# Performance work log

Measured on AMD Instinct MI355X. Metric: run time of the kernel, lower is better.

## Reference

```python
import jax, jax.numpy as jnp
import numpy as np

WD = 8        # window_dim
E = 32        # embedding_dim
D = E * WD * WD   # attention_dim = 2048
NH = 8        # num_heads (SwinTransformer default)
B, H, W = 16, 64, 64
NW = (H // WD) * (W // WD)  # 64 windows
FF = 4 * D


def _partition(x):
    # 'b (vp vw) (hp hw) e -> b (vw hw) (vp hp e)', vp=hp=WD (patches are the OUTER factor)
    b, h, w, e = x.shape
    vw, hw = h // WD, w // WD
    x = x.reshape(b, WD, vw, WD, hw, e)
    x = x.transpose(0, 2, 4, 1, 3, 5)           # b vw hw vp hp e
    return x.reshape(b, vw * hw, WD * WD * e)   # [B, NW, D]


def _layer_norm(x, g, b, eps=1e-5):
    m = jnp.mean(x, axis=-1, keepdims=True)
    v = jnp.mean(jnp.square(x - m), axis=-1, keepdims=True)
    return (x - m) * jax.lax.rsqrt(v + eps) * g + b


def setup_inputs() -> dict:
    key = jax.random.key(0)
    ks = jax.random.split(key, 8)
    s = 0.02  # weight scale to keep activations sane at D=2048
    return {
        'embeddings': jax.random.normal(ks[0], (B, H, W, E), jnp.float32),
        'ln1_g': jnp.ones((D,), jnp.float32),
        'ln1_b': jnp.zeros((D,), jnp.float32),
        'wq': jax.random.normal(ks[1], (D, D), jnp.float32) * s,
        'bq': jnp.zeros((D,), jnp.float32),
        'wk': jax.random.normal(ks[2], (D, D), jnp.float32) * s,
        'bk': jnp.zeros((D,), jnp.float32),
        'wv': jax.random.normal(ks[3], (D, D), jnp.float32) * s,
        'bv': jnp.zeros((D,), jnp.float32),
        'pos_bias': jnp.zeros((NW, NW), jnp.float32),  # source discards the randn Parameter; bias is zeros
        'ln2_g': jnp.ones((D,), jnp.float32),
        'ln2_b': jnp.zeros((D,), jnp.float32),
        'w1': jax.random.normal(ks[4], (D, FF), jnp.float32) * s,
        'b1': jnp.zeros((FF,), jnp.float32),
        'w2': jax.random.normal(ks[5], (FF, D), jnp.float32) * s,
        'b2': jnp.zeros((D,), jnp.float32),
    }


def reference(embeddings, ln1_g, ln1_b, wq, bq, wk, bk, wv, bv, pos_bias,
              ln2_g, ln2_b, w1, b1, w2, b2):
    windows = _partition(embeddings)                       # [B, NW, D]
    x = _layer_norm(windows, ln1_g, ln1_b)
    hd = D // NH

    def heads(y):  # [B, NW, D] -> [B, NH, NW, hd]  (heads are outer factor)
        return y.reshape(B, NW, NH, hd).transpose(0, 2, 1, 3)

    q = heads(x @ wq + bq)
    k = heads(x @ wk + bk)
    v = heads(x @ wv + bv)

    logits = jnp.einsum('bhnd,bhmd->bhnm', q, k) / jnp.sqrt(jnp.float32(D)) + pos_bias
    # diagonal self-attention mask (eye) applied with -inf, then softmax over keys
    diag = jnp.eye(NW, dtype=bool)
    logits = jnp.where(diag, -jnp.inf, logits)
    attn = jax.nn.softmax(logits, axis=-1)                 # [B, NH, NW, NW]

    sa = jnp.einsum('bhnm,bhmd->bhnd', attn, v)            # [B, NH, NW, hd]
    sa = sa.transpose(0, 2, 1, 3).reshape(B, NW, D)

    attn_out = windows + sa
    y = _layer_norm(attn_out, ln2_g, ln2_b)
    y = jax.nn.gelu(y @ w1 + b1, approximate=False)
    y = y @ w2 + b2
    return attn_out + y                                    # [B, NW, D]
```

## Files before the change

kernel.cpp:

```cpp
#include <hip/hip_runtime.h>
#include <math.h>

#define ROWS 1024
#define DIM  2048
#define FFDIM 8192
#define NHEAD 8
#define HD 256
#define NWIN 64
#define MB (1u << 20)

typedef __attribute__((ext_vector_type(8))) short short8;
typedef __attribute__((ext_vector_type(4))) float f32x4;
typedef unsigned int uint32;
typedef unsigned short ushort_t;

#define MFMA16(a, b, c) __builtin_amdgcn_mfma_f32_16x16x32_bf16((a), (b), (c), 0, 0, 0)
#define SWZ(r) (((r) >> 1) & 3)

__device__ __forceinline__ ushort_t rne(float x) {
  uint32 u = __float_as_uint(x);
  return (ushort_t)((u + 0x7FFFu + ((u >> 16) & 1u)) >> 16);
}
__device__ __forceinline__ float bf2f(ushort_t h) {
  return __uint_as_float(((uint32)h) << 16);
}

__global__ __launch_bounds__(256)
void wconvT_kernel(const float* __restrict__ s0, const float* __restrict__ s1,
                   const float* __restrict__ s2, ushort_t* __restrict__ d,
                   int R, int C) {
  const float* src = (blockIdx.z == 0) ? s0 : (blockIdx.z == 1) ? s1 : s2;
  ushort_t* dst = d + (size_t)blockIdx.z * R * C;
  __shared__ float tl[64][65];
  const int r0 = blockIdx.y * 64, c0 = blockIdx.x * 64;
  const int tr = threadIdx.x >> 4, tc = threadIdx.x & 15;
#pragma unroll
  for (int i = 0; i < 4; ++i) {
    const int r = tr + i * 16;
    float4 v = *(const float4*)&src[(size_t)(r0 + r) * C + c0 + tc * 4];
    tl[r][tc * 4 + 0] = v.x; tl[r][tc * 4 + 1] = v.y;
    tl[r][tc * 4 + 2] = v.z; tl[r][tc * 4 + 3] = v.w;
  }
  __syncthreads();
#pragma unroll
  for (int i = 0; i < 4; ++i) {
    const int c = tr + i * 16;
    ushort4 o;
    o.x = rne(tl[tc * 4 + 0][c]); o.y = rne(tl[tc * 4 + 1][c]);
    o.z = rne(tl[tc * 4 + 2][c]); o.w = rne(tl[tc * 4 + 3][c]);
    *(ushort4*)&dst[(size_t)(c0 + c) * R + r0 + tc * 4] = o;
  }
}

template <int MI, int EPI>
__device__ __forceinline__ void gemm_body(
    const ushort_t* __restrict__ A, const ushort_t* __restrict__ Bt,
    const float* __restrict__ bias, float* __restrict__ Cf,
    ushort_t* __restrict__ C16, int N, int K, int kbeg, int kend,
    int m0, int n0, short* As, short* Bs) {
  const int t = threadIdx.x;
  const int lane = t & 63;
  const int wid = t >> 6;
  const int wr = wid >> 1, wc = wid & 1;
  const int l15 = lane & 15, l4 = lane >> 4;
  constexpr int ACH = MI / 2;

  f32x4 acc[MI][4];
#pragma unroll
  for (int i = 0; i < MI; ++i)
#pragma unroll
    for (int j = 0; j < 4; ++j) {
      f32x4 z = {0.f, 0.f, 0.f, 0.f};
      acc[i][j] = z;
    }

  int aoff[MI], boff[4];
#pragma unroll
  for (int mi = 0; mi < MI; ++mi) {
    int m = wr * MI * 16 + mi * 16 + l15;
    aoff[mi] = m * 64 + ((l4 ^ SWZ(m)) << 4);
  }
#pragma unroll
  for (int ni = 0; ni < 4; ++ni) {
    int n = wc * 64 + ni * 16 + l15;
    boff[ni] = n * 64 + ((l4 ^ SWZ(n)) << 4);
  }

  const int srow = t >> 2, sq = t & 3;
  const ushort_t* aptr = A + (size_t)(m0 + srow) * K + sq * 8;
  const ushort_t* bptr = Bt + (size_t)(n0 + srow) * K + sq * 8;
  int awoff[ACH], bwoff[2];
#pragma unroll
  for (int j = 0; j < ACH; ++j) {
    const int row = srow + j * 64;
    awoff[j] = row * 64 + ((sq ^ SWZ(row)) << 4);
  }
#pragma unroll
  for (int j = 0; j < 2; ++j) {
    const int row = srow + j * 64;
    bwoff[j] = row * 64 + ((sq ^ SWZ(row)) << 4);
  }

  uint4 pa[ACH], pb[2];
#pragma unroll
  for (int j = 0; j < ACH; ++j)
    pa[j] = *(const uint4*)(aptr + (size_t)(j * 64) * K + kbeg);
#pragma unroll
  for (int j = 0; j < 2; ++j)
    pb[j] = *(const uint4*)(bptr + (size_t)(j * 64) * K + kbeg);

  for (int k0 = kbeg; k0 < kend; k0 += 32) {
    __syncthreads();
#pragma unroll
    for (int j = 0; j < ACH; ++j) *(uint4*)((char*)As + awoff[j]) = pa[j];
#pragma unroll
    for (int j = 0; j < 2; ++j)   *(uint4*)((char*)Bs + bwoff[j]) = pb[j];
    __syncthreads();

    if (k0 + 32 < kend) {
#pragma unroll
      for (int j = 0; j < ACH; ++j)
        pa[j] = *(const uint4*)(aptr + (size_t)(j * 64) * K + (k0 + 32));
#pragma unroll
      for (int j = 0; j < 2; ++j)
        pb[j] = *(const uint4*)(bptr + (size_t)(j * 64) * K + (k0 + 32));
    }

    short8 a[MI], b4[4];
#pragma unroll
    for (int mi = 0; mi < MI; ++mi)
      a[mi] = *(const short8*)((const char*)As + aoff[mi]);
#pragma unroll
    for (int ni = 0; ni < 4; ++ni)
      b4[ni] = *(const short8*)((const char*)Bs + boff[ni]);
#pragma unroll
    for (int mi = 0; mi < MI; ++mi)
#pragma unroll
      for (int ni = 0; ni < 4; ++ni)
        acc[mi][ni] = MFMA16(a[mi], b4[ni], acc[mi][ni]);
  }

#pragma unroll
  for (int ni = 0; ni < 4; ++ni) {
    const int n = n0 + wc * 64 + ni * 16 + l15;
    const float bb = (EPI == 3) ? 0.f : bias[n];
#pragma unroll
    for (int mi = 0; mi < MI; ++mi) {
      const int mbase = m0 + wr * MI * 16 + mi * 16 + l4 * 4;
#pragma unroll
      for (int r = 0; r < 4; ++r) {
        float x = acc[mi][ni][r] + bb;
        const size_t idx = (size_t)(mbase + r) * N + n;
        if (EPI == 0) {
          C16[idx] = rne(x);
        } else if (EPI == 1) {
          x = 0.5f * x * (1.0f + erff(x * 0.70710678118654752f));
          C16[idx] = rne(x);
        } else {
          Cf[idx] = x;
        }
      }
    }
  }
}

template <int MI, int EPI>
__global__ __launch_bounds__(256, 2)
void gemm_k(const ushort_t* __restrict__ A, const ushort_t* __restrict__ Bt,
            const float* __restrict__ bias, float* __restrict__ Cf,
            ushort_t* __restrict__ C16, int N, int K, int ksplit) {
  __shared__ __align__(16) short As[MI * 1024];
  __shared__ __align__(16) short Bs[4096];
  const int kbeg = blockIdx.z * ksplit;
  float* Cfe = (EPI == 3) ? Cf + (size_t)blockIdx.z * ROWS * N : Cf;
  gemm_body<MI, EPI>(A, Bt, bias, Cfe, C16, N, K, kbeg, kbeg + ksplit,
                     blockIdx.y * MI * 32, blockIdx.x * 128, As, Bs);
}

__global__ __launch_bounds__(256, 3)
void qkv_k(const ushort_t* __restrict__ A, const ushort_t* __restrict__ qkvT,
           const float* __restrict__ bq, const float* __restrict__ bk,
           const float* __restrict__ bv, ushort_t* __restrict__ outq) {
  __shared__ __align__(16) short As[2048];
  __shared__ __align__(16) short Bs[4096];
  const int nb = blockIdx.x;
  const int mat = nb >> 4;
  const ushort_t* W = qkvT + (size_t)mat * DIM * DIM;
  const float* B = (mat == 0) ? bq : (mat == 1) ? bk : bv;
  ushort_t* out = outq + (size_t)mat * ROWS * DIM;
  gemm_body<2, 0>(A, W, B, nullptr, out, DIM, DIM, 0, DIM,
                  blockIdx.y * 64, (nb & 15) * 128, As, Bs);
}

__global__ __launch_bounds__(256)
void reduce4_kernel(const float* __restrict__ p, const float* __restrict__ bias,
                    const float* __restrict__ R, float* __restrict__ out) {
  const int idx = blockIdx.x * 256 + threadIdx.x;
  const size_t PS = (size_t)ROWS * DIM / 4;
  const float4* p4 = (const float4*)p;
  float4 s0 = p4[idx], s1 = p4[idx + PS], s2 = p4[idx + 2 * PS], s3 = p4[idx + 3 * PS];
  const int n = (idx & (DIM / 4 - 1)) * 4;
  float4 bi = *(const float4*)&bias[n];
  float4 rr = ((const float4*)R)[idx];
  float4 o;
  o.x = s0.x + s1.x + s2.x + s3.x + bi.x + rr.x;
  o.y = s0.y + s1.y + s2.y + s3.y + bi.y + rr.y;
  o.z = s0.z + s1.z + s2.z + s3.z + bi.z + rr.z;
  o.w = s0.w + s1.w + s2.w + s3.w + bi.w + rr.w;
  ((float4*)out)[idx] = o;
}

__device__ inline void block_stats(float s, float ss, float& mean, float& rstd) {
#pragma unroll
  for (int off = 32; off; off >>= 1) {
    s  += __shfl_xor(s,  off);
    ss += __shfl_xor(ss, off);
  }
  __shared__ float red[8];
  const int t = threadIdx.x;
  const int w = t >> 6;
  if ((t & 63) == 0) { red[w] = s; red[4 | w] = ss; }
  __syncthreads();
  s  = red[0] + red[1] + red[2] + red[3];
  ss = red[4] + red[5] + red[6] + red[7];
  mean = s * (1.0f / DIM);
  float var = ss * (1.0f / DIM) - mean * mean;
  rstd = 1.0f / sqrtf(var + 1e-5f);
}

__global__ __launch_bounds__(256)
void partition_ln1_kernel(const float* __restrict__ emb,
                          const float* __restrict__ g, const float* __restrict__ be,
                          float* __restrict__ windows, ushort_t* __restrict__ xbf) {
  const int row = blockIdx.x;
  const int b = row >> 6, n = row & 63;
  const int vw = n >> 3, hw = n & 7;
  const int t = threadIdx.x;
  const int d0 = t * 4, d1 = d0 + 1024;

  const int vp0 = d0 >> 8, hp0 = (d0 >> 5) & 7, e0 = d0 & 31;
  const int vp1 = d1 >> 8, hp1 = (d1 >> 5) & 7, e1 = d1 & 31;
  float4 v0 = *(const float4*)&emb[(size_t)(((b*64 + vp0*8 + vw)*64) + hp0*8 + hw)*32 + e0];
  float4 v1 = *(const float4*)&emb[(size_t)(((b*64 + vp1*8 + vw)*64) + hp1*8 + hw)*32 + e1];

  float s  = v0.x+v0.y+v0.z+v0.w + v1.x+v1.y+v1.z+v1.w;
  float ss = v0.x*v0.x+v0.y*v0.y+v0.z*v0.z+v0.w*v0.w
           + v1.x*v1.x+v1.y*v1.y+v1.z*v1.z+v1.w*v1.w;
  float mean, rstd;
  block_stats(s, ss, mean, rstd);

  float* wrow = windows + (size_t)row * DIM;
  *(float4*)&wrow[d0] = v0;
  *(float4*)&wrow[d1] = v1;

  float4 g0 = *(const float4*)&g[d0],  g1 = *(const float4*)&g[d1];
  float4 b0 = *(const float4*)&be[d0], b1 = *(const float4*)&be[d1];
  ushort4 o0, o1;
  o0.x = rne((v0.x-mean)*rstd*g0.x + b0.x); o0.y = rne((v0.y-mean)*rstd*g0.y + b0.y);
  o0.z = rne((v0.z-mean)*rstd*g0.z + b0.z); o0.w = rne((v0.w-mean)*rstd*g0.w + b0.w);
  o1.x = rne((v1.x-mean)*rstd*g1.x + b1.x); o1.y = rne((v1.y-mean)*rstd*g1.y + b1.y);
  o1.z = rne((v1.z-mean)*rstd*g1.z + b1.z); o1.w = rne((v1.w-mean)*rstd*g1.w + b1.w);
  *(ushort4*)&xbf[(size_t)row * DIM + d0] = o0;
  *(ushort4*)&xbf[(size_t)row * DIM + d1] = o1;
}

__global__ __launch_bounds__(256)
void ln_kernel(const float* __restrict__ in, const float* __restrict__ g,
               const float* __restrict__ be, ushort_t* __restrict__ out) {
  const int row = blockIdx.x;
  const int t = threadIdx.x;
  const float* x = in + (size_t)row * DIM;
  const int d0 = t * 4, d1 = d0 + 1024;
  float4 v0 = *(const float4*)&x[d0];
  float4 v1 = *(const float4*)&x[d1];
  float s  = v0.x+v0.y+v0.z+v0.w + v1.x+v1.y+v1.z+v1.w;
  float ss = v0.x*v0.x+v0.y*v0.y+v0.z*v0.z+v0.w*v0.w
           + v1.x*v1.x+v1.y*v1.y+v1.z*v1.z+v1.w*v1.w;
  float mean, rstd;
  block_stats(s, ss, mean, rstd);
  float4 g0 = *(const float4*)&g[d0],  g1 = *(const float4*)&g[d1];
  float4 b0 = *(const float4*)&be[d0], b1 = *(const float4*)&be[d1];
  ushort4 o0, o1;
  o0.x = rne((v0.x-mean)*rstd*g0.x + b0.x); o0.y = rne((v0.y-mean)*rstd*g0.y + b0.y);
  o0.z = rne((v0.z-mean)*rstd*g0.z + b0.z); o0.w = rne((v0.w-mean)*rstd*g0.w + b0.w);
  o1.x = rne((v1.x-mean)*rstd*g1.x + b1.x); o1.y = rne((v1.y-mean)*rstd*g1.y + b1.y);
  o1.z = rne((v1.z-mean)*rstd*g1.z + b1.z); o1.w = rne((v1.w-mean)*rstd*g1.w + b1.w);
  *(ushort4*)&out[(size_t)row * DIM + d0] = o0;
  *(ushort4*)&out[(size_t)row * DIM + d1] = o1;
}

__global__ __launch_bounds__(256)
void attn_kernel(const ushort_t* __restrict__ Q, const ushort_t* __restrict__ K,
                 const ushort_t* __restrict__ V, const float* __restrict__ pb,
                 const float* __restrict__ windows, float* __restrict__ attn_out) {
  __shared__ __align__(16) float kv[NWIN][264];
  __shared__ __align__(16) float qs[32][268];
  __shared__ float att[32][NWIN + 1];
  const int blk = blockIdx.x;
  const int bh = blk >> 1, half = blk & 1;
  const int b = bh >> 3, h = bh & 7;
  const int qbase = half * 32;
  const int t = threadIdx.x;
  const size_t base = (size_t)b * 64 * DIM + (size_t)h * HD;

#pragma unroll
  for (int j = 0; j < 8; ++j) {
    int idx = t + j * 256;
    int m = idx >> 5, c8 = idx & 31;
    uint4 raw = *(const uint4*)&K[base + (size_t)m * DIM + c8 * 8];
    float4 f0 = {bf2f((ushort_t)(raw.x & 0xffff)), bf2f((ushort_t)(raw.x >> 16)),
                 bf2f((ushort_t)(raw.y & 0xffff)), bf2f((ushort_t)(raw.y >> 16))};
    float4 f1 = {bf2f((ushort_t)(raw.z & 0xffff)), bf2f((ushort_t)(raw.z >> 16)),
                 bf2f((ushort_t)(raw.w & 0xffff)), bf2f((ushort_t)(raw.w >> 16))};
    *(float4*)&kv[m][c8 * 8] = f0;
    *(float4*)&kv[m][c8 * 8 + 4] = f1;
  }
#pragma unroll
  for (int j = 0; j < 4; ++j) {
    int idx = t + j * 256;
    int m = idx >> 5, c8 = idx & 31;
    uint4 raw = *(const uint4*)&Q[base + (size_t)(qbase + m) * DIM + c8 * 8];
    float4 f0 = {bf2f((ushort_t)(raw.x & 0xffff)), bf2f((ushort_t)(raw.x >> 16)),
                 bf2f((ushort_t)(raw.y & 0xffff)), bf2f((ushort_t)(raw.y >> 16))};
    float4 f1 = {bf2f((ushort_t)(raw.z & 0xffff)), bf2f((ushort_t)(raw.z >> 16)),
                 bf2f((ushort_t)(raw.w & 0xffff)), bf2f((ushort_t)(raw.w >> 16))};
    *(float4*)&qs[m][c8 * 8] = f0;
    *(float4*)&qs[m][c8 * 8 + 4] = f1;
  }
  __syncthreads();

  {
    const int rp = t & 15;
    const int kg = t >> 4;
    float acc[2][4] = {};
    for (int dg = 0; dg < 64; ++dg) {
      float4 q0 = *(const float4*)&qs[rp][dg * 4];
      float4 q1 = *(const float4*)&qs[rp + 16][dg * 4];
#pragma unroll
      for (int j = 0; j < 4; ++j) {
        float4 kr = *(const float4*)&kv[4 * kg + j][dg * 4];
        acc[0][j] += q0.x * kr.x + q0.y * kr.y + q0.z * kr.z + q0.w * kr.w;
        acc[1][j] += q1.x * kr.x + q1.y * kr.y + q1.z * kr.z + q1.w * kr.w;
      }
    }
    const float scale = 0.022097086912079608f;
#pragma unroll
    for (int i = 0; i < 2; ++i) {
      const int rl = rp + i * 16;
      const int gr = qbase + rl;
#pragma unroll
      for (int j = 0; j < 4; ++j) {
        const int m = 4 * kg + j;
        float l = acc[i][j] * scale + pb[gr * 64 + m];
        if (m == gr) l = -INFINITY;
        att[rl][m] = l;
      }
    }
  }
  __syncthreads();

#pragma unroll
  for (int j = 0; j < 8; ++j) {
    int idx = t + j * 256;
    int m = idx >> 5, c8 = idx & 31;
    uint4 raw = *(const uint4*)&V[base + (size_t)m * DIM + c8 * 8];
    float4 f0 = {bf2f((ushort_t)(raw.x & 0xffff)), bf2f((ushort_t)(raw.x >> 16)),
                 bf2f((ushort_t)(raw.y & 0xffff)), bf2f((ushort_t)(raw.y >> 16))};
    float4 f1 = {bf2f((ushort_t)(raw.z & 0xffff)), bf2f((ushort_t)(raw.z >> 16)),
                 bf2f((ushort_t)(raw.w & 0xffff)), bf2f((ushort_t)(raw.w >> 16))};
    *(float4*)&kv[m][c8 * 8] = f0;
    *(float4*)&kv[m][c8 * 8 + 4] = f1;
  }
  if (t < 32) {
    float mx = -INFINITY;
#pragma unroll
    for (int m = 0; m < 64; ++m) mx = fmaxf(mx, att[t][m]);
    float sum = 0.f;
#pragma unroll
    for (int m = 0; m < 64; ++m) {
      float e = expf(att[t][m] - mx);
      att[t][m] = e;
      sum += e;
    }
    float inv = 1.0f / sum;
#pragma unroll
    for (int m = 0; m < 64; ++m) att[t][m] *= inv;
  }
  __syncthreads();

  {
    const int dg = t & 63, rg = t >> 6;
    float4 s[8];
#pragma unroll
    for (int i = 0; i < 8; ++i) s[i] = make_float4(0.f, 0.f, 0.f, 0.f);
    for (int m = 0; m < 64; ++m) {
      float4 vr = *(const float4*)&kv[m][dg * 4];
#pragma unroll
      for (int i = 0; i < 8; ++i) {
        const float a = att[rg * 8 + i][m];
        s[i].x = fmaf(a, vr.x, s[i].x); s[i].y = fmaf(a, vr.y, s[i].y);
        s[i].z = fmaf(a, vr.z, s[i].z); s[i].w = fmaf(a, vr.w, s[i].w);
      }
    }
#pragma unroll
    for (int i = 0; i < 8; ++i) {
      const int row = qbase + rg * 8 + i;
      const size_t o = base + (size_t)row * DIM + dg * 4;
      float4 w4 = *(const float4*)&windows[o];
      float4 r;
      r.x = s[i].x + w4.x; r.y = s[i].y + w4.y;
      r.z = s[i].z + w4.z; r.w = s[i].w + w4.w;
      *(float4*)&attn_out[o] = r;
    }
  }
}

extern "C" void kernel_launch(void* const* d_in, const int* in_sizes, int n_in,
                              void* d_out, int out_size, void* d_ws, size_t ws_size,
                              hipStream_t stream) {
  const float* emb  = (const float*)d_in[0];
  const float* ln1g = (const float*)d_in[1];
  const float* ln1b = (const float*)d_in[2];
  const float* wq   = (const float*)d_in[3];
  const float* bq   = (const float*)d_in[4];
  const float* wk   = (const float*)d_in[5];
  const float* bk   = (const float*)d_in[6];
  const float* wv   = (const float*)d_in[7];
  const float* bv   = (const float*)d_in[8];
  const float* pb   = (const float*)d_in[9];
  const float* ln2g = (const float*)d_in[10];
  const float* ln2b = (const float*)d_in[11];
  const float* w1   = (const float*)d_in[12];
  const float* b1   = (const float*)d_in[13];
  const float* w2   = (const float*)d_in[14];
  const float* b2   = (const float*)d_in[15];
  float* out = (float*)d_out;

  char* W8 = (char*)d_ws;
  float*    windows  = (float*)(W8 + (size_t)0 * MB);
  ushort_t* xbf      = (ushort_t*)(W8 + (size_t)8 * MB);
  ushort_t* w1T      = (ushort_t*)(W8 + (size_t)12 * MB);
  ushort_t* qb       = (ushort_t*)(W8 + (size_t)44 * MB);
  float*    attn_out = (float*)(W8 + (size_t)56 * MB);
  ushort_t* qkvT     = (ushort_t*)(W8 + (size_t)64 * MB);
  ushort_t* w2T      = (ushort_t*)(W8 + (size_t)64 * MB);
  ushort_t* ffh      = (ushort_t*)(W8 + (size_t)96 * MB);
  float*    partial  = (float*)(W8 + (size_t)0 * MB);
  const size_t OFF = (size_t)ROWS * DIM;

  wconvT_kernel<<<dim3(32, 32, 3), 256, 0, stream>>>(wq, wk, wv, qkvT, DIM, DIM);
  wconvT_kernel<<<dim3(128, 32, 1), 256, 0, stream>>>(w1, w1, w1, w1T, DIM, FFDIM);

  partition_ln1_kernel<<<ROWS, 256, 0, stream>>>(emb, ln1g, ln1b, windows, xbf);

  qkv_k<<<dim3(48, 16), 256, 0, stream>>>(xbf, qkvT, bq, bk, bv, qb);

  attn_kernel<<<16 * NHEAD * 2, 256, 0, stream>>>(qb, qb + OFF, qb + 2 * OFF, pb,
                                                  windows, attn_out);

  wconvT_kernel<<<dim3(32, 128, 1), 256, 0, stream>>>(w2, w2, w2, w2T, FFDIM, DIM);

  ln_kernel<<<ROWS, 256, 0, stream>>>(attn_out, ln2g, ln2b, xbf);

  gemm_k<4, 1><<<dim3(64, 8, 1), 256, 0, stream>>>(
      xbf, w1T, b1, nullptr, ffh, FFDIM, DIM, DIM);
  gemm_k<4, 3><<<dim3(16, 8, 4), 256, 0, stream>>>(
      ffh, w2T, nullptr, partial, nullptr, DIM, FFDIM, FFDIM / 4);
  reduce4_kernel<<<(ROWS * DIM / 4) / 256, 256, 0, stream>>>(partial, b2, attn_out, out);
}
```

Baseline: 655.7 us.

## Use direct global-to-LDS loads with double buffering and swizzled block order in GEMMs

The GEMM body is rewritten to load A/B tiles with global_load_lds straight into LDS, replacing the register-staged loads and XOR swizzle. It double-buffers LDS so only one barrier is needed per K step. The FFN GEMMs shrink to 64-row tiles (MI=2) with more blocks and higher occupancy, and all three GEMM kernels use a 1D grid remapped by an XCD-aware swizzle for cache locality. The unswizzled LDS layout may cause bank conflicts, and the smaller tiles reduce reuse per block.

```diff
diff --git a/kernel.cpp b/kernel.cpp
--- a/kernel.cpp
+++ b/kernel.cpp
@@ -15,7 +15,11 @@
 typedef unsigned short ushort_t;
 
 #define MFMA16(a, b, c) __builtin_amdgcn_mfma_f32_16x16x32_bf16((a), (b), (c), 0, 0, 0)
-#define SWZ(r) (((r) >> 1) & 3)
+
+#define GLOAD(g, l)                                                          \
+  __builtin_amdgcn_global_load_lds(                                          \
+      (const __attribute__((address_space(1))) unsigned int*)(g),            \
+      (__attribute__((address_space(3))) unsigned int*)(l), 16, 0, 0)
 
 __device__ __forceinline__ ushort_t rne(float x) {
   uint32 u = __float_as_uint(x);
@@ -24,120 +28,71 @@
 __device__ __forceinline__ float bf2f(ushort_t h) {
   return __uint_as_float(((uint32)h) << 16);
 }
-
-__global__ __launch_bounds__(256)
-void wconvT_kernel(const float* __restrict__ s0, const float* __restrict__ s1,
-                   const float* __restrict__ s2, ushort_t* __restrict__ d,
-                   int R, int C) {
-  const float* src = (blockIdx.z == 0) ? s0 : (blockIdx.z == 1) ? s1 : s2;
-  ushort_t* dst = d + (size_t)blockIdx.z * R * C;
-  __shared__ float tl[64][65];
-  const int r0 = blockIdx.y * 64, c0 = blockIdx.x * 64;
-  const int tr = threadIdx.x >> 4, tc = threadIdx.x & 15;
-#pragma unroll
-  for (int i = 0; i < 4; ++i) {
-    const int r = tr + i * 16;
-    float4 v = *(const float4*)&src[(size_t)(r0 + r) * C + c0 + tc * 4];
-    tl[r][tc * 4 + 0] = v.x; tl[r][tc * 4 + 1] = v.y;
-    tl[r][tc * 4 + 2] = v.z; tl[r][tc * 4 + 3] = v.w;
-  }
-  __syncthreads();
-#pragma unroll
-  for (int i = 0; i < 4; ++i) {
-    const int c = tr + i * 16;
-    ushort4 o;
-    o.x = rne(tl[tc * 4 + 0][c]); o.y = rne(tl[tc * 4 + 1][c]);
-    o.z = rne(tl[tc * 4 + 2][c]); o.w = rne(tl[tc * 4 + 3][c]);
-    *(ushort4*)&dst[(size_t)(c0 + c) * R + r0 + tc * 4] = o;
-  }
-}
-
-template <int MI, int EPI>
-__device__ __forceinline__ void gemm_body(
+__device__ __forceinline__ int swz8(int id, int nwg) {
+  const int c = nwg >> 3;
+  return (id & 7) * c + (id >> 3);
+}
+
+template <int EPI>
+__device__ __forceinline__ void gbody(
     const ushort_t* __restrict__ A, const ushort_t* __restrict__ Bt,
     const float* __restrict__ bias, float* __restrict__ Cf,
     ushort_t* __restrict__ C16, int N, int K, int kbeg, int kend,
     int m0, int n0, short* As, short* Bs) {
   const int t = threadIdx.x;
-  const int lane = t & 63;
-  const int wid = t >> 6;
+  const int lane = t & 63, wid = t >> 6;
   const int wr = wid >> 1, wc = wid & 1;
   const int l15 = lane & 15, l4 = lane >> 4;
-  constexpr int ACH = MI / 2;
-
-  f32x4 acc[MI][4];
-#pragma unroll
-  for (int i = 0; i < MI; ++i)
+
+  f32x4 acc[2][4];
+#pragma unroll
+  for (int i = 0; i < 2; ++i)
 #pragma unroll
     for (int j = 0; j < 4; ++j) {
       f32x4 z = {0.f, 0.f, 0.f, 0.f};
       acc[i][j] = z;
     }
 
-  int aoff[MI], boff[4];
-#pragma unroll
-  for (int mi = 0; mi < MI; ++mi) {
-    int m = wr * MI * 16 + mi * 16 + l15;
-    aoff[mi] = m * 64 + ((l4 ^ SWZ(m)) << 4);
-  }
-#pragma unroll
-  for (int ni = 0; ni < 4; ++ni) {
-    int n = wc * 64 + ni * 16 + l15;
-    boff[ni] = n * 64 + ((l4 ^ SWZ(n)) << 4);
-  }
-
-  const int srow = t >> 2, sq = t & 3;
-  const ushort_t* aptr = A + (size_t)(m0 + srow) * K + sq * 8;
-  const ushort_t* bptr = Bt + (size_t)(n0 + srow) * K + sq * 8;
-  int awoff[ACH], bwoff[2];
-#pragma unroll
-  for (int j = 0; j < ACH; ++j) {
-    const int row = srow + j * 64;
-    awoff[j] = row * 64 + ((sq ^ SWZ(row)) << 4);
-  }
-#pragma unroll
-  for (int j = 0; j < 2; ++j) {
-    const int row = srow + j * 64;
-    bwoff[j] = row * 64 + ((sq ^ SWZ(row)) << 4);
-  }
-
-  uint4 pa[ACH], pb[2];
-#pragma unroll
-  for (int j = 0; j < ACH; ++j)
-    pa[j] = *(const uint4*)(aptr + (size_t)(j * 64) * K + kbeg);
-#pragma unroll
-  for (int j = 0; j < 2; ++j)
-    pb[j] = *(const uint4*)(bptr + (size_t)(j * 64) * K + kbeg);
-
-  for (int k0 = kbeg; k0 < kend; k0 += 32) {
+  const int abase = l4 * 1024 + (wr * 32 + l15) * 16;
+  const int bbase = l4 * 2048 + (wc * 64 + l15) * 16;
+
+  const ushort_t* ga  = A  + (size_t)(m0 + lane) * K + wid * 8;
+  const ushort_t* gb0 = Bt + (size_t)(n0 + lane) * K + wid * 8;
+  const ushort_t* gb1 = Bt + (size_t)(n0 + 64 + lane) * K + wid * 8;
+
+  const int nt = (kend - kbeg) >> 5;
+
+  GLOAD(ga + kbeg, As + wid * 512);
+  GLOAD(gb0 + kbeg, Bs + (wid * 2) * 512);
+  GLOAD(gb1 + kbeg, Bs + (wid * 2 + 1) * 512);
+  __syncthreads();
+
+  for (int tt = 0; tt < nt; ++tt) {
+    short* Ac = As + (tt & 1) * 2048;
+    short* Bc = Bs + (tt & 1) * 4096;
+    if (tt + 1 < nt) {
+      const int kn = kbeg + (tt + 1) * 32;
+      short* An = As + ((tt + 1) & 1) * 2048;
+      short* Bn = Bs + ((tt + 1) & 1) * 4096;
+      GLOAD(ga + kn, An + wid * 512);
+      GLOAD(gb0 + kn, Bn + (wid * 2) * 512);
+      GLOAD(gb1 + kn, Bn + (wid * 2 + 1) * 512);
+    }
+    short8 a0 = *(const short8*)((const char*)Ac + abase);
+    short8 a1 = *(const short8*)((const char*)Ac + abase + 256);
+    short8 b0 = *(const short8*)((const char*)Bc + bbase);
+    short8 b1 = *(const short8*)((const char*)Bc + bbase + 256);
+    short8 b2 = *(const short8*)((const char*)Bc + bbase + 512);
+    short8 b3 = *(const short8*)((const char*)Bc + bbase + 768);
+    acc[0][0] = MFMA16(a0, b0, acc[0][0]);
+    acc[0][1] = MFMA16(a0, b1, acc[0][1]);
+    acc[0][2] = MFMA16(a0, b2, acc[0][2]);
+    acc[0][3] = MFMA16(a0, b3, acc[0][3]);
+    acc[1][0] = MFMA16(a1, b0, acc[1][0]);
+    acc[1][1] = MFMA16(a1, b1, acc[1][1]);
+    acc[1][2] = MFMA16(a1, b2, acc[1][2]);
+    acc[1][3] = MFMA16(a1, b3, acc[1][3]);
     __syncthreads();
-#pragma unroll
-    for (int j = 0; j < ACH; ++j) *(uint4*)((char*)As + awoff[j]) = pa[j];
-#pragma unroll
-    for (int j = 0; j < 2; ++j)   *(uint4*)((char*)Bs + bwoff[j]) = pb[j];
-    __syncthreads();
-
-    if (k0 + 32 < kend) {
-#pragma unroll
-      for (int j = 0; j < ACH; ++j)
-        pa[j] = *(const uint4*)(aptr + (size_t)(j * 64) * K + (k0 + 32));
-#pragma unroll
-      for (int j = 0; j < 2; ++j)
-        pb[j] = *(const uint4*)(bptr + (size_t)(j * 64) * K + (k0 + 32));
-    }
-
-    short8 a[MI], b4[4];
-#pragma unroll
-    for (int mi = 0; mi < MI; ++mi)
-      a[mi] = *(const short8*)((const char*)As + aoff[mi]);
-#pragma unroll
-    for (int ni = 0; ni < 4; ++ni)
-      b4[ni] = *(const short8*)((const char*)Bs + boff[ni]);
-#pragma unroll
-    for (int mi = 0; mi < MI; ++mi)
-#pragma unroll
-      for (int ni = 0; ni < 4; ++ni)
-        acc[mi][ni] = MFMA16(a[mi], b4[ni], acc[mi][ni]);
   }
 
 #pragma unroll
@@ -145,8 +100,8 @@
     const int n = n0 + wc * 64 + ni * 16 + l15;
     const float bb = (EPI == 3) ? 0.f : bias[n];
 #pragma unroll
-    for (int mi = 0; mi < MI; ++mi) {
-      const int mbase = m0 + wr * MI * 16 + mi * 16 + l4 * 4;
+    for (int mi = 0; mi < 2; ++mi) {
+      const int mbase = m0 + wr * 32 + mi * 16 + l4 * 4;
 #pragma unroll
       for (int r = 0; r < 4; ++r) {
         float x = acc[mi][ni][r] + bb;
@@ -164,32 +119,69 @@
   }
 }
 
-template <int MI, int EPI>
-__global__ __launch_bounds__(256, 2)
-void gemm_k(const ushort_t* __restrict__ A, const ushort_t* __restrict__ Bt,
-            const float* __restrict__ bias, float* __restrict__ Cf,
-            ushort_t* __restrict__ C16, int N, int K, int ksplit) {
-  __shared__ __align__(16) short As[MI * 1024];
-  __shared__ __align__(16) short Bs[4096];
-  const int kbeg = blockIdx.z * ksplit;
-  float* Cfe = (EPI == 3) ? Cf + (size_t)blockIdx.z * ROWS * N : Cf;
-  gemm_body<MI, EPI>(A, Bt, bias, Cfe, C16, N, K, kbeg, kbeg + ksplit,
-                     blockIdx.y * MI * 32, blockIdx.x * 128, As, Bs);
-}
-
-__global__ __launch_bounds__(256, 3)
-void qkv_k(const ushort_t* __restrict__ A, const ushort_t* __restrict__ qkvT,
-           const float* __restrict__ bq, const float* __restrict__ bk,
-           const float* __restrict__ bv, ushort_t* __restrict__ outq) {
-  __shared__ __align__(16) short As[2048];
-  __shared__ __align__(16) short Bs[4096];
-  const int nb = blockIdx.x;
-  const int mat = nb >> 4;
+__global__ __launch_bounds__(256, 4)
+void qkv2_k(const ushort_t* __restrict__ A, const ushort_t* __restrict__ qkvT,
+            const float* __restrict__ bq, const float* __restrict__ bk,
+            const float* __restrict__ bv, ushort_t* __restrict__ outq) {
+  __shared__ __align__(16) short As[2 * 2048];
+  __shared__ __align__(16) short Bs[2 * 4096];
+  const int id = swz8(blockIdx.x, 768);
+  const int mat = id >> 8, r = id & 255;
+  const int m0 = ((r >> 4) & 15) * 64, n0 = (r & 15) * 128;
   const ushort_t* W = qkvT + (size_t)mat * DIM * DIM;
-  const float* B = (mat == 0) ? bq : (mat == 1) ? bk : bv;
+  const float* bias = (mat == 0) ? bq : (mat == 1) ? bk : bv;
   ushort_t* out = outq + (size_t)mat * ROWS * DIM;
-  gemm_body<2, 0>(A, W, B, nullptr, out, DIM, DIM, 0, DIM,
-                  blockIdx.y * 64, (nb & 15) * 128, As, Bs);
+  gbody<0>(A, W, bias, nullptr, out, DIM, DIM, 0, DIM, m0, n0, As, Bs);
+}
+
+__global__ __launch_bounds__(256, 4)
+void ffn1_k(const ushort_t* __restrict__ A, const ushort_t* __restrict__ w1T,
+            const float* __restrict__ b1, ushort_t* __restrict__ ffh) {
+  __shared__ __align__(16) short As[2 * 2048];
+  __shared__ __align__(16) short Bs[2 * 4096];
+  const int id = swz8(blockIdx.x, 1024);
+  const int m0 = (id >> 6) * 64, n0 = (id & 63) * 128;
+  gbody<1>(A, w1T, b1, nullptr, ffh, FFDIM, DIM, 0, DIM, m0, n0, As, Bs);
+}
+
+__global__ __launch_bounds__(256, 4)
+void ffn2_k(const ushort_t* __restrict__ ffh, const ushort_t* __restrict__ w2T,
+            float* __restrict__ partial) {
+  __shared__ __align__(16) short As[2 * 2048];
+  __shared__ __align__(16) short Bs[2 * 4096];
+  const int id = swz8(blockIdx.x, 1024);
+  const int ks = id >> 8, r = id & 255;
+  const int m0 = ((r >> 4) & 15) * 64, n0 = (r & 15) * 128;
+  float* Cf = partial + (size_t)ks * ROWS * DIM;
+  gbody<3>(ffh, w2T, nullptr, Cf, nullptr, DIM, FFDIM, ks * 2048,
+           ks * 2048 + 2048, m0, n0, As, Bs);
+}
+
+__global__ __launch_bounds__(256)
+void wconvT_kernel(const float* __restrict__ s0, const float* __restrict__ s1,
+                   const float* __restrict__ s2, ushort_t* __restrict__ d,
+                   int R, int C) {
+  const float* src = (blockIdx.z == 0) ? s0 : (blockIdx.z == 1) ? s1 : s2;
+  ushort_t* dst = d + (size_t)blockIdx.z * R * C;
+  __shared__ float tl[64][65];
+  const int r0 = blockIdx.y * 64, c0 = blockIdx.x * 64;
+  const int tr = threadIdx.x >> 4, tc = threadIdx.x & 15;
+#pragma unroll
+  for (int i = 0; i < 4; ++i) {
+    const int r = tr + i * 16;
+    float4 v = *(const float4*)&src[(size_t)(r0 + r) * C + c0 + tc * 4];
+    tl[r][tc * 4 + 0] = v.x; tl[r][tc * 4 + 1] = v.y;
+    tl[r][tc * 4 + 2] = v.z; tl[r][tc * 4 + 3] = v.w;
+  }
+  __syncthreads();
+#pragma unroll
+  for (int i = 0; i < 4; ++i) {
+    const int c = tr + i * 16;
+    ushort4 o;
+    o.x = rne(tl[tc * 4 + 0][c]); o.y = rne(tl[tc * 4 + 1][c]);
+    o.z = rne(tl[tc * 4 + 2][c]); o.w = rne(tl[tc * 4 + 3][c]);
+    *(ushort4*)&dst[(size_t)(c0 + c) * R + r0 + tc * 4] = o;
+  }
 }
 
 __global__ __launch_bounds__(256)
@@ -453,7 +445,7 @@
 
   partition_ln1_kernel<<<ROWS, 256, 0, stream>>>(emb, ln1g, ln1b, windows, xbf);
 
-  qkv_k<<<dim3(48, 16), 256, 0, stream>>>(xbf, qkvT, bq, bk, bv, qb);
+  qkv2_k<<<768, 256, 0, stream>>>(xbf, qkvT, bq, bk, bv, qb);
 
   attn_kernel<<<16 * NHEAD * 2, 256, 0, stream>>>(qb, qb + OFF, qb + 2 * OFF, pb,
                                                   windows, attn_out);
@@ -462,9 +454,7 @@
 
   ln_kernel<<<ROWS, 256, 0, stream>>>(attn_out, ln2g, ln2b, xbf);
 
-  gemm_k<4, 1><<<dim3(64, 8, 1), 256, 0, stream>>>(
-      xbf, w1T, b1, nullptr, ffh, FFDIM, DIM, DIM);
-  gemm_k<4, 3><<<dim3(16, 8, 4), 256, 0, stream>>>(
-      ffh, w2T, nullptr, partial, nullptr, DIM, FFDIM, FFDIM / 4);
+  ffn1_k<<<1024, 256, 0, stream>>>(xbf, w1T, b1, ffh);
+  ffn2_k<<<1024, 256, 0, stream>>>(ffh, w2T, partial);
   reduce4_kernel<<<(ROWS * DIM / 4) / 256, 256, 0, stream>>>(partial, b2, attn_out, out);
 }
```

Measured after the change: 544.4 us. 1.2x faster.
